# Performance work log

Hardware: AMD Instinct MI355X
Metric: run time of the kernel (lower is better)

The kernel has to match this reference:

```python
import jax, jax.numpy as jnp
import numpy as np

NUM_HEADS = 16
ROPE_THETA = 10000.0


def _apply_rope(x):
    # x: (b, h, n, d). Interleaved-pair RoPE as in rotary_embedding_torch
    d = x.shape[-1]
    n = x.shape[-2]
    inv_freq = 1.0 / (ROPE_THETA ** (jnp.arange(0, d, 2, dtype=jnp.float32) / d))
    t = jnp.arange(n, dtype=jnp.float32)
    freqs = t[:, None] * inv_freq[None, :]            # (n, d/2)
    freqs = jnp.repeat(freqs, 2, axis=-1)             # (n, d) interleaved
    cos = jnp.cos(freqs).astype(x.dtype)
    sin = jnp.sin(freqs).astype(x.dtype)
    xp = x.reshape(*x.shape[:-1], d // 2, 2)
    x_rot = jnp.stack((-xp[..., 1], xp[..., 0]), axis=-1).reshape(x.shape)
    return x * cos + x_rot * sin


def _attention(x_q, x_k, x_v, W_q, W_k, W_v, W_out, padding_mask, is_causal, start_pos):
    b, n, hidden = x_q.shape
    h = NUM_HEADS
    d = hidden // h
    # torch Linear (no bias): y = x @ W.T
    q = (x_q @ W_q.T).reshape(b, n, h, d).transpose(0, 2, 1, 3)  # (b,h,n,d)
    k = (x_k @ W_k.T).reshape(b, n, h, d).transpose(0, 2, 1, 3)
    v = (x_v @ W_v.T).reshape(b, n, h, d).transpose(0, 2, 1, 3)
    q = _apply_rope(q)
    k = _apply_rope(k)
    # combined mask, built via broadcasting instead of a dense (b,1,n,n) tensor
    i = jnp.arange(n)[:, None]
    j = jnp.arange(n)[None, :]
    if is_causal:
        # allowed: key before start_pos always visible; otherwise causal tril
        allow = (j < start_pos) | ((i >= start_pos) & (i >= j))  # (n,n)
    else:
        allow = jnp.ones((n, n), dtype=bool)
    mask = allow[None, None, :, :] & padding_mask[:, None, None, :]  # (b,1,n,n)
    scale = 1.0 / jnp.sqrt(jnp.asarray(d, dtype=q.dtype))
    scores = jnp.einsum('bhqd,bhkd->bhqk', q, k) * scale
    scores = jnp.where(mask, scores, jnp.asarray(-jnp.inf, dtype=scores.dtype))
    attn = jax.nn.softmax(scores, axis=-1)
    out = jnp.einsum('bhqk,bhkd->bhqd', attn, v)
    out = out.transpose(0, 2, 1, 3).reshape(b, n, hidden)
    return out @ W_out.T


def setup_inputs() -> dict:
    key = jax.random.key(0)
    ks = jax.random.split(key, 7)
    b, n, hidden = 4, 2048, 1024
    s = 1.0 / np.sqrt(hidden)
    return {
        'x_q': jax.random.normal(ks[0], (b, n, hidden), dtype=jnp.float32),
        'x_k': jax.random.normal(ks[1], (b, n, hidden), dtype=jnp.float32),
        'x_v': jax.random.normal(ks[2], (b, n, hidden), dtype=jnp.float32),
        'W_q': jax.random.normal(ks[3], (hidden, hidden), dtype=jnp.float32) * s,
        'W_k': jax.random.normal(ks[4], (hidden, hidden), dtype=jnp.float32) * s,
        'W_v': jax.random.normal(ks[5], (hidden, hidden), dtype=jnp.float32) * s,
        'W_out': jax.random.normal(ks[6], (hidden, hidden), dtype=jnp.float32) * s,
        'padding_mask': jnp.ones((b, n), dtype=bool),
        'is_causal': 1,
        'start_pos': 0,
    }


def reference(x_q, x_k, x_v, W_q, W_k, W_v, W_out, padding_mask, is_causal, start_pos):
    return _attention(x_q, x_k, x_v, W_q, W_k, W_v, W_out, padding_mask, is_causal, start_pos)
```

## Files before the change

kernel.cpp:

```cpp
#include <hip/hip_runtime.h>
#include <hip/hip_bf16.h>
#include <math.h>

#define BB 4
#define SEQ 2048
#define HEADS 16
#define DH 64
#define HID 1024
#define MM (BB*SEQ)
#define KK HID

typedef __attribute__((ext_vector_type(8))) short bf16x8;
typedef __attribute__((ext_vector_type(4))) float f32x4;
typedef __attribute__((ext_vector_type(16))) float f32x16;
typedef unsigned short u16;
typedef unsigned int u32;

__device__ __forceinline__ u16 f2bf(float f){
  u32 u = __builtin_bit_cast(u32, f);
  u += 0x7fffu + ((u>>16)&1u);
  return (u16)(u>>16);
}

__device__ __forceinline__ uint4 pack8(const float4 a, const float4 b){
  uint4 r;
  r.x = (u32)f2bf(a.x) | ((u32)f2bf(a.y)<<16);
  r.y = (u32)f2bf(a.z) | ((u32)f2bf(a.w)<<16);
  r.z = (u32)f2bf(b.x) | ((u32)f2bf(b.y)<<16);
  r.w = (u32)f2bf(b.z) | ((u32)f2bf(b.w)<<16);
  return r;
}

#define MFMA(a,b,c)   __builtin_amdgcn_mfma_f32_16x16x32_bf16(a,b,c,0,0,0)
#define MFMA32(a,b,c) __builtin_amdgcn_mfma_f32_32x32x16_bf16(a,b,c,0,0,0)

__device__ __forceinline__ void gload16(const u16* g, u16* l){
  __builtin_amdgcn_global_load_lds(
    (const __attribute__((address_space(1))) unsigned int*)(const void*)g,
    (__attribute__((address_space(3))) unsigned int*)(void*)l, 16, 0, 0);
}

__global__ void rope_tab_kernel(float2* tab){
  int idx = blockIdx.x*256 + threadIdx.x;
  if (idx >= SEQ*32) return;
  int pos = idx >> 5, p = idx & 31;
  double inv = exp2(-(double)p * (13.287712379549449/32.0));
  double a = (double)pos * inv;
  tab[idx] = make_float2((float)cos(a), (float)sin(a));
}

__global__ __launch_bounds__(1024)
void mask_bias_kernel(const int* pm, float* bias, u32* flagbits, int nelem){
  __shared__ int flag;
  if (threadIdx.x == 0) flag = 0;
  if (threadIdx.x < BB) flagbits[threadIdx.x] = 0u;
  __syncthreads();
  int bad = 0;
  for (int i = threadIdx.x; i < nelem/4; i += 1024){
    u32 v = ((const u32*)pm)[i];
    if (v > 1u) bad = 1;
  }
  if (bad) atomicOr(&flag, 1);
  __syncthreads();
  const int u8mode = flag;
  for (int i = threadIdx.x; i < nelem; i += 1024){
    int v = u8mode ? (int)((const unsigned char*)pm)[i] : pm[i];
    bias[i] = v ? 0.f : -__builtin_inff();
    if (!v) atomicOr(&flagbits[i>>11], 1u << ((i & (SEQ-1)) >> 6));
  }
}

template<int MODE>
__global__ __launch_bounds__(256,2)
void gemm_k(const void* Ap, const float* W, void* outp, const float2* tab)
{
  constexpr int BK = 32;
  __shared__ u16 lA[128][40];
  __shared__ u16 lB[128][40];
  const int tid  = threadIdx.x;
  const int lane = tid & 63;
  const int wid  = tid >> 6;
  const int wr = wid >> 1, wc = wid & 1;
  const int bm = blockIdx.x, bn = blockIdx.y;
  const int arow0 = bm*128, brow0 = bn*128;

  f32x4 acc[4][4];
  #pragma unroll
  for (int i=0;i<4;i++)
    #pragma unroll
    for (int j=0;j<4;j++) acc[i][j] = (f32x4){0.f,0.f,0.f,0.f};

  const int sr = tid >> 2;
  const int sc = tid & 3;

  const float* Af = (const float*)Ap;
  const u16*   Ab = (const u16*)Ap;

  float4 ra[2][2], rb[2][2];
  uint4  rab[2];

  auto loadA = [&](int k0){
    if constexpr (MODE==3){
      const u16* p = Ab + (size_t)(arow0 + (tid>>1))*KK + k0 + (tid&1)*16;
      rab[0] = *(const uint4*)(p);
      rab[1] = *(const uint4*)(p+8);
    } else {
      #pragma unroll
      for (int s=0;s<2;s++){
        const float* p = Af + (size_t)(arow0 + sr + s*64)*KK + k0 + sc*8;
        ra[s][0] = *(const float4*)p;
        ra[s][1] = *(const float4*)(p+4);
      }
    }
  };
  auto loadB = [&](int k0){
    #pragma unroll
    for (int s=0;s<2;s++){
      const float* p = W + (size_t)(brow0 + sr + s*64)*KK + k0 + sc*8;
      rb[s][0] = *(const float4*)p;
      rb[s][1] = *(const float4*)(p+4);
    }
  };

  loadA(0); loadB(0);

  for (int t=0; t<KK/BK; ++t){
    __syncthreads();
    if constexpr (MODE==3){
      *(uint4*)&lA[tid>>1][(tid&1)*16 + 0] = rab[0];
      *(uint4*)&lA[tid>>1][(tid&1)*16 + 8] = rab[1];
    } else {
      *(uint4*)&lA[sr   ][sc*8] = pack8(ra[0][0], ra[0][1]);
      *(uint4*)&lA[sr+64][sc*8] = pack8(ra[1][0], ra[1][1]);
    }
    *(uint4*)&lB[sr   ][sc*8] = pack8(rb[0][0], rb[0][1]);
    *(uint4*)&lB[sr+64][sc*8] = pack8(rb[1][0], rb[1][1]);
    __syncthreads();
    if (t+1 < KK/BK){ loadA((t+1)*BK); loadB((t+1)*BK); }

    bf16x8 af[4], bfr[4];
    const int g = lane >> 4, rr = lane & 15;
    #pragma unroll
    for (int i=0;i<4;i++) af[i]  = *(const bf16x8*)&lA[wr*64 + i*16 + rr][g*8];
    #pragma unroll
    for (int j=0;j<4;j++) bfr[j] = *(const bf16x8*)&lB[wc*64 + j*16 + rr][g*8];
    #pragma unroll
    for (int i=0;i<4;i++)
      #pragma unroll
      for (int j=0;j<4;j++)
        acc[i][j] = MFMA(af[i], bfr[j], acc[i][j]);
  }

  #pragma unroll
  for (int i=0;i<4;i++){
    #pragma unroll
    for (int j=0;j<4;j++){
      if constexpr (MODE==2){
        const int m0 = arow0 + wr*64 + i*16 + (lane>>4)*4;
        const int c  = brow0 + wc*64 + j*16 + (lane&15);
        const int pos = m0 & (SEQ-1);
        const int bidx = m0 >> 11;
        const int h = c >> 6, dd = c & 63;
        uint2 pk;
        pk.x = (u32)f2bf(acc[i][j][0]) | ((u32)f2bf(acc[i][j][1])<<16);
        pk.y = (u32)f2bf(acc[i][j][2]) | ((u32)f2bf(acc[i][j][3])<<16);
        *(uint2*)&((u16*)outp)[((size_t)(bidx*HEADS + h)*DH + dd)*SEQ + pos] = pk;
      } else {
        #pragma unroll
        for (int r=0;r<4;r++){
          const int m = arow0 + wr*64 + i*16 + (lane>>4)*4 + r;
          const int c = brow0 + wc*64 + j*16 + (lane&15);
          float v = acc[i][j][r];
          if constexpr (MODE==3){
            ((float*)outp)[(size_t)m*HID + c] = v;
          } else {
            const int pos = m & (SEQ-1);
            const int bidx = m >> 11;
            const int h = c >> 6, dd = c & 63;
            float2 cs = tab[pos*32 + (dd>>1)];
            float vp = __shfl_xor(v, 1);
            float o = ((dd&1)==0) ? (v*cs.x - vp*cs.y) : (v*cs.x + vp*cs.y);
            if constexpr (MODE==0) o *= 0.18033688011112042f;
            ((u16*)outp)[(((size_t)(bidx*HEADS + h))*SEQ + pos)*DH + dd] = f2bf(o);
          }
        }
      }
    }
  }
}

__global__ __launch_bounds__(256,3)
void attn_k(const u16* q, const u16* kkp, const u16* vtp, u16* o,
            const float* bias_g, const u32* flagbits, const int* pcaus, const int* psp)
{
  const int tid = threadIdx.x, lane = tid & 63, wid = tid >> 6;
  const int NQT = SEQ/64;
  const int q0lo = blockIdx.x*64;
  const int q0hi = (NQT-1-(int)blockIdx.x)*64;
  const int bh = blockIdx.y, b = bh >> 4;
  const int causal = *pcaus, sp = *psp;

  __shared__ u16 lK[2][64*64];
  __shared__ u16 lV[2][64*64];

  const size_t hbase = (size_t)bh * SEQ * DH;
  const int h = lane >> 5, ln31 = lane & 31, ln7 = lane & 7;

  const int i0w = (wid < 2) ? (q0lo + wid*32) : (q0hi + (wid-2)*32);
  const int myq = i0w + ln31;
  const u32 fbits = flagbits[b];

  bf16x8 qf[4];
  {
    const u16* qr = q + hbase + (size_t)myq*DH;
    #pragma unroll
    for (int s=0;s<4;s++) qf[s] = *(const bf16x8*)(qr + 16*s + 8*h);
  }

  int swz[4];
  #pragma unroll
  for (int s=0;s<4;s++) swz[s] = ((2*s + h) ^ ln7) * 8;

  f32x16 oac[2];
  #pragma unroll
  for (int t=0;t<16;t++){ oac[0][t] = 0.f; oac[1][t] = 0.f; }
  float mrun = -__builtin_inff(), lrun = 0.f;

  int jmax = causal ? ((q0hi+63 > sp-1) ? q0hi+63 : sp-1) : (SEQ-1);
  if (jmax > SEQ-1) jmax = SEQ-1;
  const int ntile = (jmax >> 6) + 1;

  auto stage = [&](int buf, int kt){
    const int j0 = kt*64;
    #pragma unroll
    for (int c=0;c<2;c++){
      const int row = wid*16 + c*8 + (lane>>3);
      const int sl  = (ln7 ^ (lane>>3)) * 8;
      gload16(kkp + hbase + (size_t)(j0+row)*DH + sl, &lK[buf][(wid*16+c*8)*64]);
      gload16(vtp + hbase + (size_t)row*SEQ + j0 + sl, &lV[buf][(wid*16+c*8)*64]);
    }
  };

  stage(0, 0);
  __syncthreads();
  int cur = 0;

  for (int kt=0; kt<ntile; ++kt){
    const int j0 = kt*64;
    if (kt+1 < ntile) stage(cur^1, kt+1);

    const bool active = !(causal && j0 >= sp && j0 > i0w+31);
    if (active){
      const u16* Kb = lK[cur];
      const u16* Vb = lV[cur];

      f32x16 sA, sB;
      #pragma unroll
      for (int t=0;t<16;t++){ sA[t] = 0.f; sB[t] = 0.f; }
      __builtin_amdgcn_s_setprio(1);
      #pragma unroll
      for (int s=0;s<4;s++){
        bf16x8 k0 = *(const bf16x8*)&Kb[ ln31    *64 + swz[s]];
        bf16x8 k1 = *(const bf16x8*)&Kb[(32+ln31)*64 + swz[s]];
        sA = MFMA32(k0, qf[s], sA);
        sB = MFMA32(k1, qf[s], sB);
      }
      __builtin_amdgcn_s_setprio(0);

      float sv[32];
      #pragma unroll
      for (int t=0;t<16;t++){ sv[t] = sA[t]; sv[16+t] = sB[t]; }

      if ((fbits >> kt) & 1u){
        #pragma unroll
        for (int t=0;t<32;t++){
          const int rt = ((t&3) + 8*((t&15)>>2) + 4*h) + 32*(t>>4);
          sv[t] += bias_g[b*SEQ + j0 + rt];
        }
      }
      const bool needmask = causal && !((j0+63 < sp) || (i0w >= sp && j0+63 <= i0w));
      if (needmask){
        #pragma unroll
        for (int t=0;t<32;t++){
          const int jj = j0 + ((t&3) + 8*((t&15)>>2) + 4*h) + 32*(t>>4);
          const bool allow = (jj < sp) || (myq >= sp && myq >= jj);
          sv[t] = allow ? sv[t] : -__builtin_inff();
        }
      }

      float m8[8];
      #pragma unroll
      for (int t=0;t<8;t++)
        m8[t] = fmaxf(fmaxf(sv[t], sv[t+8]), fmaxf(sv[t+16], sv[t+24]));
      float m4a = fmaxf(fmaxf(m8[0],m8[1]), fmaxf(m8[2],m8[3]));
      float m4b = fmaxf(fmaxf(m8[4],m8[5]), fmaxf(m8[6],m8[7]));
      float pmax = fmaxf(m4a, m4b);
      pmax = fmaxf(pmax, __shfl_xor(pmax, 32));
      const float mnew = fmaxf(mrun, pmax);
      if (!__all(pmax - mrun <= 8.f)){
        const float fac = exp2f(mrun - mnew);
        mrun = mnew;
        lrun *= fac;
        oac[0] *= fac;
        oac[1] *= fac;
      }
      float p[32];
      #pragma unroll
      for (int t=0;t<32;t++) p[t] = exp2f(sv[t] - mrun);
      float a16[16];
      #pragma unroll
      for (int t=0;t<16;t++) a16[t] = p[t] + p[t+16];
      float a8[8];
      #pragma unroll
      for (int t=0;t<8;t++) a8[t] = a16[t] + a16[t+8];
      float rs = ((a8[0]+a8[1]) + (a8[2]+a8[3])) + ((a8[4]+a8[5]) + (a8[6]+a8[7]));
      rs += __shfl_xor(rs, 32);
      lrun += rs;

      u32 w[16];
      #pragma unroll
      for (int u=0;u<16;u++){
        asm("v_cvt_pk_bf16_f32 %0, %1, %2" : "=v"(w[u]) : "v"(p[2*u]), "v"(p[2*u+1]));
      }

      __builtin_amdgcn_s_setprio(1);
      #pragma unroll
      for (int st=0; st<4; ++st){
        const int base = 8*(st>>1) + 4*(st&1);
        u32 x0 = h ? w[base+0] : w[base+2];
        u32 x1 = h ? w[base+1] : w[base+3];
        u32 r0 = (u32)__shfl_xor((int)x0, 32);
        u32 r1 = (u32)__shfl_xor((int)x1, 32);
        uint4 fw;
        fw.x = h ? r0 : w[base+0];
        fw.y = h ? r1 : w[base+1];
        fw.z = h ? w[base+2] : r0;
        fw.w = h ? w[base+3] : r1;
        bf16x8 pf = __builtin_bit_cast(bf16x8, fw);
        #pragma unroll
        for (int dt=0; dt<2; ++dt){
          bf16x8 vf = *(const bf16x8*)&Vb[(dt*32+ln31)*64 + swz[st]];
          oac[dt] = MFMA32(vf, pf, oac[dt]);
        }
      }
      __builtin_amdgcn_s_setprio(0);
    }

    __syncthreads();
    cur ^= 1;
  }

  const float inv = 1.f / lrun;
  u16* orow = o + ((size_t)(b*SEQ) + myq)*HID + (size_t)(bh&15)*DH;
  #pragma unroll
  for (int dt=0; dt<2; ++dt)
    #pragma unroll
    for (int a=0; a<4; ++a){
      const int d0 = dt*32 + 8*a + 4*h;
      uint2 pk;
      pk.x = (u32)f2bf(oac[dt][4*a+0]*inv) | ((u32)f2bf(oac[dt][4*a+1]*inv)<<16);
      pk.y = (u32)f2bf(oac[dt][4*a+2]*inv) | ((u32)f2bf(oac[dt][4*a+3]*inv)<<16);
      *(uint2*)(orow + d0) = pk;
    }
}

extern "C" void kernel_launch(void* const* d_in, const int* in_sizes, int n_in,
                              void* d_out, int out_size, void* d_ws, size_t ws_size,
                              hipStream_t stream)
{
  const float* x_q = (const float*)d_in[0];
  const float* x_k = (const float*)d_in[1];
  const float* x_v = (const float*)d_in[2];
  const float* W_q = (const float*)d_in[3];
  const float* W_k = (const float*)d_in[4];
  const float* W_v = (const float*)d_in[5];
  const float* W_o = (const float*)d_in[6];
  const int*   pm  = (const int*)d_in[7];
  const int* caus = (const int*)d_in[8];
  const int* sp   = (const int*)d_in[9];

  char* ws = (char*)d_ws;
  float2* tab   = (float2*)ws;
  u16*  v_ws    = (u16*)(ws + (1u<<20));
  u16*  o_ws    = (u16*)(ws + (17u<<20));
  float* bias   = (float*)(ws + (33u<<20));
  u32*  flagb   = (u32*)(ws + (33u<<20) + (1u<<15));
  u16* q_ws = (u16*)d_out;
  u16* k_ws = ((u16*)d_out) + (size_t)MM*HID;

  rope_tab_kernel<<<SEQ*32/256, 256, 0, stream>>>(tab);
  mask_bias_kernel<<<1, 1024, 0, stream>>>(pm, bias, flagb, BB*SEQ);

  dim3 gg(MM/128, HID/128);
  gemm_k<0><<<gg, 256, 0, stream>>>(x_q, W_q, q_ws, tab);
  gemm_k<1><<<gg, 256, 0, stream>>>(x_k, W_k, k_ws, tab);
  gemm_k<2><<<gg, 256, 0, stream>>>(x_v, W_v, v_ws, tab);

  dim3 ga(SEQ/128, BB*HEADS);
  attn_k<<<ga, 256, 0, stream>>>(q_ws, k_ws, v_ws, o_ws, bias, flagb, caus, sp);

  gemm_k<3><<<gg, 256, 0, stream>>>(o_ws, W_o, d_out, tab);
}
```

Measured before the change: 303.5 us.

## Pre-convert weights to bf16 and stream B tiles via global_load_lds double buffering

Adds a kernel that converts all four fp32 weight matrices to bf16 once per call in workspace. The GEMMs then stage bf16 B tiles straight into a double-buffered LDS region with global_load_lds, which halves weight traffic and removes the per-tile register pack step. It also raises the attention kernel's launch-bounds occupancy hint from 3 to 4 blocks. The cost is an extra conversion kernel and more LDS use, and the fast path only runs when the workspace is large enough.

```diff
diff --git a/kernel.cpp b/kernel.cpp
--- a/kernel.cpp
+++ b/kernel.cpp
@@ -47,6 +47,18 @@
   double inv = exp2(-(double)p * (13.287712379549449/32.0));
   double a = (double)pos * inv;
   tab[idx] = make_float2((float)cos(a), (float)sin(a));
+}
+
+__global__ __launch_bounds__(256)
+void w2bf_kernel(const float* w0, const float* w1, const float* w2,
+                 const float* w3, u16* dst){
+  const int idx = blockIdx.x*256 + threadIdx.x;
+  const float* srcs[4] = {w0, w1, w2, w3};
+  const int which = idx >> 17;
+  const int off = (idx & 131071) * 8;
+  const float4* s = (const float4*)(srcs[which] + off);
+  float4 a = s[0], b = s[1];
+  *(uint4*)(dst + (size_t)which*(KK*KK) + off) = pack8(a, b);
 }
 
 __global__ __launch_bounds__(1024)
@@ -70,13 +82,15 @@
   }
 }
 
-template<int MODE>
+template<int MODE, int WB>
 __global__ __launch_bounds__(256,2)
-void gemm_k(const void* Ap, const float* W, void* outp, const float2* tab)
+void gemm_k(const void* Ap, const void* Wp, void* outp, const float2* tab)
 {
   constexpr int BK = 32;
   __shared__ u16 lA[128][40];
-  __shared__ u16 lB[128][40];
+  __shared__ u16 lB[2][128][32];
+  u16 (*lBo)[40] = (u16(*)[40])&lB[0][0][0];
+
   const int tid  = threadIdx.x;
   const int lane = tid & 63;
   const int wid  = tid >> 6;
@@ -95,6 +109,8 @@
 
   const float* Af = (const float*)Ap;
   const u16*   Ab = (const u16*)Ap;
+  const float* Wf = (const float*)Wp;
+  const u16*   Wb = (const u16*)Wp;
 
   float4 ra[2][2], rb[2][2];
   uint4  rab[2];
@@ -116,13 +132,22 @@
   auto loadB = [&](int k0){
     #pragma unroll
     for (int s=0;s<2;s++){
-      const float* p = W + (size_t)(brow0 + sr + s*64)*KK + k0 + sc*8;
+      const float* p = Wf + (size_t)(brow0 + sr + s*64)*KK + k0 + sc*8;
       rb[s][0] = *(const float4*)p;
       rb[s][1] = *(const float4*)(p+4);
     }
   };
-
-  loadA(0); loadB(0);
+  auto stageB = [&](int buf, int k0){
+    #pragma unroll
+    for (int s=0;s<2;s++){
+      const u16* p = Wb + (size_t)(brow0 + s*64 + (tid>>2))*KK + k0 + (tid&3)*8;
+      gload16(p, &lB[buf][s*64 + (tid>>2)][(tid&3)*8]);
+    }
+  };
+
+  loadA(0);
+  if constexpr (WB) stageB(0, 0); else loadB(0);
+  int bcur = 0;
 
   for (int t=0; t<KK/BK; ++t){
     __syncthreads();
@@ -133,22 +158,31 @@
       *(uint4*)&lA[sr   ][sc*8] = pack8(ra[0][0], ra[0][1]);
       *(uint4*)&lA[sr+64][sc*8] = pack8(ra[1][0], ra[1][1]);
     }
-    *(uint4*)&lB[sr   ][sc*8] = pack8(rb[0][0], rb[0][1]);
-    *(uint4*)&lB[sr+64][sc*8] = pack8(rb[1][0], rb[1][1]);
+    if constexpr (!WB){
+      *(uint4*)&lBo[sr   ][sc*8] = pack8(rb[0][0], rb[0][1]);
+      *(uint4*)&lBo[sr+64][sc*8] = pack8(rb[1][0], rb[1][1]);
+    }
     __syncthreads();
-    if (t+1 < KK/BK){ loadA((t+1)*BK); loadB((t+1)*BK); }
+    if (t+1 < KK/BK){
+      loadA((t+1)*BK);
+      if constexpr (WB) stageB(bcur^1, (t+1)*BK); else loadB((t+1)*BK);
+    }
 
     bf16x8 af[4], bfr[4];
     const int g = lane >> 4, rr = lane & 15;
     #pragma unroll
-    for (int i=0;i<4;i++) af[i]  = *(const bf16x8*)&lA[wr*64 + i*16 + rr][g*8];
-    #pragma unroll
-    for (int j=0;j<4;j++) bfr[j] = *(const bf16x8*)&lB[wc*64 + j*16 + rr][g*8];
+    for (int i=0;i<4;i++) af[i] = *(const bf16x8*)&lA[wr*64 + i*16 + rr][g*8];
+    #pragma unroll
+    for (int j=0;j<4;j++){
+      if constexpr (WB) bfr[j] = *(const bf16x8*)&lB[bcur][wc*64 + j*16 + rr][g*8];
+      else              bfr[j] = *(const bf16x8*)&lBo[wc*64 + j*16 + rr][g*8];
+    }
     #pragma unroll
     for (int i=0;i<4;i++)
       #pragma unroll
       for (int j=0;j<4;j++)
         acc[i][j] = MFMA(af[i], bfr[j], acc[i][j]);
+    bcur ^= 1;
   }
 
   #pragma unroll
@@ -189,7 +223,7 @@
   }
 }
 
-__global__ __launch_bounds__(256,3)
+__global__ __launch_bounds__(256,4)
 void attn_k(const u16* q, const u16* kkp, const u16* vtp, u16* o,
             const float* bias_g, const u32* flagbits, const int* pcaus, const int* psp)
 {
@@ -385,6 +419,10 @@
   u16*  o_ws    = (u16*)(ws + (17u<<20));
   float* bias   = (float*)(ws + (33u<<20));
   u32*  flagb   = (u32*)(ws + (33u<<20) + (1u<<15));
+  u16*  wbf     = (u16*)(ws + (34u<<20));
+  const size_t NEED = (34u<<20) + (size_t)4*KK*KK*2;
+  const bool WBOK = ws_size >= NEED;
+
   u16* q_ws = (u16*)d_out;
   u16* k_ws = ((u16*)d_out) + (size_t)MM*HID;
 
@@ -392,12 +430,20 @@
   mask_bias_kernel<<<1, 1024, 0, stream>>>(pm, bias, flagb, BB*SEQ);
 
   dim3 gg(MM/128, HID/128);
-  gemm_k<0><<<gg, 256, 0, stream>>>(x_q, W_q, q_ws, tab);
-  gemm_k<1><<<gg, 256, 0, stream>>>(x_k, W_k, k_ws, tab);
-  gemm_k<2><<<gg, 256, 0, stream>>>(x_v, W_v, v_ws, tab);
-
   dim3 ga(SEQ/128, BB*HEADS);
-  attn_k<<<ga, 256, 0, stream>>>(q_ws, k_ws, v_ws, o_ws, bias, flagb, caus, sp);
-
-  gemm_k<3><<<gg, 256, 0, stream>>>(o_ws, W_o, d_out, tab);
-}
+
+  if (WBOK){
+    w2bf_kernel<<<2048, 256, 0, stream>>>(W_q, W_k, W_v, W_o, wbf);
+    gemm_k<0,1><<<gg, 256, 0, stream>>>(x_q, wbf,                q_ws, tab);
+    gemm_k<1,1><<<gg, 256, 0, stream>>>(x_k, wbf + (size_t)KK*KK,   k_ws, tab);
+    gemm_k<2,1><<<gg, 256, 0, stream>>>(x_v, wbf + (size_t)2*KK*KK, v_ws, tab);
+    attn_k<<<ga, 256, 0, stream>>>(q_ws, k_ws, v_ws, o_ws, bias, flagb, caus, sp);
+    gemm_k<3,1><<<gg, 256, 0, stream>>>(o_ws, wbf + (size_t)3*KK*KK, d_out, tab);
+  } else {
+    gemm_k<0,0><<<gg, 256, 0, stream>>>(x_q, W_q, q_ws, tab);
+    gemm_k<1,0><<<gg, 256, 0, stream>>>(x_k, W_k, k_ws, tab);
+    gemm_k<2,0><<<gg, 256, 0, stream>>>(x_v, W_v, v_ws, tab);
+    attn_k<<<ga, 256, 0, stream>>>(q_ws, k_ws, v_ws, o_ws, bias, flagb, caus, sp);
+    gemm_k<3,0><<<gg, 256, 0, stream>>>(o_ws, W_o, d_out, tab);
+  }
+}
```

Result: no change. 309.5 us (+2.0%).

## Stage K/V tiles through registers instead of direct global-to-LDS loads

Applied to the files above, without the earlier changes.

Replaces the direct global_load_lds async copies in the attention kernel with register-staged loads: the next K/V tile is fetched into registers before compute and written to the swizzled LDS buffer afterward, with a single barrier per iteration at loop top. The launch-bounds occupancy hint is also raised from 3 to 4 blocks per SM. The aim is to overlap global latency with MFMA work and increase occupancy, at the cost of extra VGPRs for staging and possible register pressure or spills under the tighter bound.

```diff
diff --git a/kernel.cpp b/kernel.cpp
--- a/kernel.cpp
+++ b/kernel.cpp
@@ -33,12 +33,6 @@
 
 #define MFMA(a,b,c)   __builtin_amdgcn_mfma_f32_16x16x32_bf16(a,b,c,0,0,0)
 #define MFMA32(a,b,c) __builtin_amdgcn_mfma_f32_32x32x16_bf16(a,b,c,0,0,0)
-
-__device__ __forceinline__ void gload16(const u16* g, u16* l){
-  __builtin_amdgcn_global_load_lds(
-    (const __attribute__((address_space(1))) unsigned int*)(const void*)g,
-    (__attribute__((address_space(3))) unsigned int*)(void*)l, 16, 0, 0);
-}
 
 __global__ void rope_tab_kernel(float2* tab){
   int idx = blockIdx.x*256 + threadIdx.x;
@@ -189,7 +183,7 @@
   }
 }
 
-__global__ __launch_bounds__(256,3)
+__global__ __launch_bounds__(256,4)
 void attn_k(const u16* q, const u16* kkp, const u16* vtp, u16* o,
             const float* bias_g, const u32* flagbits, const int* pcaus, const int* psp)
 {
@@ -230,24 +224,32 @@
   if (jmax > SEQ-1) jmax = SEQ-1;
   const int ntile = (jmax >> 6) + 1;
 
-  auto stage = [&](int buf, int kt){
+  uint4 kr0, kr1, vr0, vr1;
+  const int srow = tid >> 2;
+  const int sg   = (tid & 3)*2;
+  const int sw   = srow & 7;
+  auto gload = [&](int kt){
     const int j0 = kt*64;
-    #pragma unroll
-    for (int c=0;c<2;c++){
-      const int row = wid*16 + c*8 + (lane>>3);
-      const int sl  = (ln7 ^ (lane>>3)) * 8;
-      gload16(kkp + hbase + (size_t)(j0+row)*DH + sl, &lK[buf][(wid*16+c*8)*64]);
-      gload16(vtp + hbase + (size_t)row*SEQ + j0 + sl, &lV[buf][(wid*16+c*8)*64]);
-    }
+    const u16* pk = kkp + hbase + (size_t)(j0+srow)*DH + sg*8;
+    kr0 = *(const uint4*)pk;  kr1 = *(const uint4*)(pk+8);
+    const u16* pv = vtp + hbase + (size_t)srow*SEQ + j0 + sg*8;
+    vr0 = *(const uint4*)pv;  vr1 = *(const uint4*)(pv+8);
   };
-
-  stage(0, 0);
-  __syncthreads();
+  auto lwrite = [&](int buf){
+    *(uint4*)&lK[buf][srow*64 + ((sg    ^sw)*8)] = kr0;
+    *(uint4*)&lK[buf][srow*64 + (((sg+1)^sw)*8)] = kr1;
+    *(uint4*)&lV[buf][srow*64 + ((sg    ^sw)*8)] = vr0;
+    *(uint4*)&lV[buf][srow*64 + (((sg+1)^sw)*8)] = vr1;
+  };
+
+  gload(0);
+  lwrite(0);
   int cur = 0;
 
   for (int kt=0; kt<ntile; ++kt){
     const int j0 = kt*64;
-    if (kt+1 < ntile) stage(cur^1, kt+1);
+    __syncthreads();
+    if (kt+1 < ntile) gload(kt+1);
 
     const bool active = !(causal && j0 >= sp && j0 > i0w+31);
     if (active){
@@ -346,7 +348,7 @@
       __builtin_amdgcn_s_setprio(0);
     }
 
-    __syncthreads();
+    if (kt+1 < ntile) lwrite(cur^1);
     cur ^= 1;
   }
 
```

New measurement: 325.1 us. +7.1%, slower.
